# Performance work log

Measured on AMD Instinct MI355X. Metric: run time of the kernel, lower is better.

Reference implementation:

```python
import jax, jax.numpy as jnp
import numpy as np

N_NODES = 100000
N_EDGES = 1200000
IN_DIM, HID_DIM, OUT_DIM = 64, 64, 32


def setup_inputs() -> dict:
    key = jax.random.key(0)
    k1, k2, k3, k4, k5, k6 = jax.random.split(key, 6)
    x = jax.random.normal(k1, (N_NODES, IN_DIM), dtype=jnp.float32)
    edge_index = jax.random.randint(k2, (2, N_EDGES), 0, N_NODES, dtype=jnp.int64)
    # Glorot-style init for GCN linear weights
    W1 = jax.random.normal(k3, (IN_DIM, HID_DIM), dtype=jnp.float32) / np.sqrt(IN_DIM)
    b1 = jnp.zeros((HID_DIM,), dtype=jnp.float32)
    W2 = jax.random.normal(k4, (HID_DIM, OUT_DIM), dtype=jnp.float32) / np.sqrt(HID_DIM)
    b2 = jnp.zeros((OUT_DIM,), dtype=jnp.float32)
    return {"x": x, "edge_index": edge_index, "W1": W1, "b1": b1, "W2": W2, "b2": b2}


def _gcn_conv(x, W, b, src, dst, norm, n_nodes):
    # linear transform first (PyG GCNConv): [N, out]
    h = x @ W
    # gather messages along edges (incl. self-loops), scale by sym norm
    msg = h[src] * norm[:, None]            # [E+N, out]
    out = jax.ops.segment_sum(msg, dst, num_segments=n_nodes)
    return out + b


def reference(x, edge_index, W1, b1, W2, b2):
    n_nodes = x.shape[0]
    # add self-loops (PyG GCNConv default)
    loop = jnp.arange(n_nodes, dtype=edge_index.dtype)
    src = jnp.concatenate([edge_index[0], loop])
    dst = jnp.concatenate([edge_index[1], loop])
    # symmetric normalization: deg^{-1/2}[src] * deg^{-1/2}[dst]
    deg = jax.ops.segment_sum(jnp.ones_like(dst, dtype=x.dtype), dst, num_segments=n_nodes)
    deg_isqrt = jax.lax.rsqrt(deg)          # deg >= 1 due to self-loops
    norm = deg_isqrt[src] * deg_isqrt[dst]
    h = _gcn_conv(x, W1, b1, src, dst, norm, n_nodes)
    h = jax.nn.relu(h)
    out = _gcn_conv(h, W2, b2, src, dst, norm, n_nodes)
    return out
```

## Files before the change

kernel.cpp:

```cpp
#include <hip/hip_runtime.h>
#include <hip/hip_fp16.h>
#include <type_traits>

#define NBUCK 512

typedef _Float16 half8 __attribute__((ext_vector_type(8)));
typedef float floatx4 __attribute__((ext_vector_type(4)));

__device__ inline void unpack8(const float4& raw, float* f) {
    const __half2* p = (const __half2*)&raw;
#pragma unroll
    for (int i = 0; i < 4; ++i) {
        float2 t = __half22float2(p[i]);
        f[2 * i] = t.x;
        f[2 * i + 1] = t.y;
    }
}


__global__ void bucket_hist_kernel(const int* __restrict__ dst, int* __restrict__ bucketCnt,
                                   int E, int R) {
    __shared__ int h[NBUCK];
    int tid = threadIdx.x;
    for (int i = tid; i < NBUCK; i += blockDim.x) h[i] = 0;
    __syncthreads();
    for (int i = blockIdx.x * blockDim.x + tid; i < E; i += gridDim.x * blockDim.x)
        atomicAdd(&h[dst[i] / R], 1);
    __syncthreads();
    for (int i = tid; i < NBUCK; i += blockDim.x)
        if (h[i]) atomicAdd(&bucketCnt[i], h[i]);
}


__global__ void bucket_scan_kernel(const int* __restrict__ bucketCnt, int* __restrict__ bucketBase,
                                   int* __restrict__ bucketCursor) {
    __shared__ int lds[NBUCK];
    int tid = threadIdx.x;
    int v = bucketCnt[tid];
    lds[tid] = v;
    __syncthreads();
    for (int off = 1; off < NBUCK; off <<= 1) {
        int x = (tid >= off) ? lds[tid - off] : 0;
        __syncthreads();
        lds[tid] += x;
        __syncthreads();
    }
    int excl = lds[tid] - v;
    bucketBase[tid] = excl;
    bucketCursor[tid] = excl;
    if (tid == NBUCK - 1) bucketBase[NBUCK] = lds[tid];
}


__global__ __launch_bounds__(1024) void partition_kernel(const int* __restrict__ src,
                                                         const int* __restrict__ dst,
                                                         int* __restrict__ bucketCursor,
                                                         unsigned long long* __restrict__ pairs,
                                                         int E, int R) {
    __shared__ int h[NBUCK];
    __shared__ int base[NBUCK];
    __shared__ int lcur[NBUCK];
    const int CH = 16384;
    int start = blockIdx.x * CH;
    int count = E - start;
    if (count > CH) count = CH;
    int tid = threadIdx.x;
    if (tid < NBUCK) h[tid] = 0;
    __syncthreads();
    for (int i = tid; i < count; i += 1024)
        atomicAdd(&h[dst[start + i] / R], 1);
    __syncthreads();
    if (tid < NBUCK) {
        base[tid] = h[tid] ? atomicAdd(&bucketCursor[tid], h[tid]) : 0;
        lcur[tid] = 0;
    }
    __syncthreads();
    for (int i = tid; i < count; i += 1024) {
        int d = dst[start + i];
        int s = src[start + i];
        int b = d / R;
        int r = atomicAdd(&lcur[b], 1);
        pairs[base[b] + r] = ((unsigned long long)(unsigned)s << 32) | (unsigned)d;
    }
}


__global__ void bucket_csr_kernel(const unsigned long long* __restrict__ pairs,
                                  const int* __restrict__ bucketBase, int* __restrict__ counts,
                                  int* __restrict__ offs, float* __restrict__ dinv,
                                  int* __restrict__ ssrc, int N, int R) {
    __shared__ int h[256];
    __shared__ int loffs[256];
    __shared__ int cur[256];
    int b = blockIdx.x, tid = threadIdx.x;
    int nodeBase = b * R;
    int beg = bucketBase[b], end = bucketBase[b + 1];
    h[tid] = 0;
    __syncthreads();
    for (int i = beg + tid; i < end; i += 256) {
        int d = (int)(pairs[i] & 0xffffffffull);
        atomicAdd(&h[d - nodeBase], 1);
    }
    __syncthreads();
    int v = h[tid];
    loffs[tid] = v;
    __syncthreads();
    for (int off = 1; off < 256; off <<= 1) {
        int x = (tid >= off) ? loffs[tid - off] : 0;
        __syncthreads();
        loffs[tid] += x;
        __syncthreads();
    }
    int excl = loffs[tid] - v;
    cur[tid] = excl;
    int node = nodeBase + tid;
    if (tid < R && node < N) {
        counts[node] = v;
        offs[node] = beg + excl;
        dinv[node] = rsqrtf((float)v + 1.0f);
    }
    __syncthreads();
    for (int i = beg + tid; i < end; i += 256) {
        unsigned long long p = pairs[i];
        int d = (int)(p & 0xffffffffull);
        int s = (int)(p >> 32);
        int r = atomicAdd(&cur[d - nodeBase], 1);
        ssrc[beg + r] = s;
    }
}


template <int OUTD, typename TIN>
__global__ void gemm_mfma_kernel(const TIN* __restrict__ X, const float* __restrict__ W,
                                 __half* __restrict__ H, int M, int ntiles) {
    constexpr int NC = OUTD / 16;
    const int lane = threadIdx.x & 63;
    const int wid  = threadIdx.x >> 6;
    const int q    = lane >> 4;
    const int m    = lane & 15;

    half8 bfrag[2][NC];
#pragma unroll
    for (int s = 0; s < 2; ++s)
#pragma unroll
        for (int c = 0; c < NC; ++c)
#pragma unroll
            for (int j = 0; j < 8; ++j)
                bfrag[s][c][j] = (_Float16)W[(s * 32 + q * 8 + j) * OUTD + c * 16 + m];

    for (int tile = blockIdx.x * 4 + wid; tile < ntiles; tile += gridDim.x * 4) {
        int rowBase = tile * 16;
        int rowA = rowBase + m;
        if (rowA > M - 1) rowA = M - 1;

        half8 afrag[2];
        if constexpr (std::is_same<TIN, float>::value) {
            const float4* Xr = (const float4*)(X + (size_t)rowA * 64);
#pragma unroll
            for (int s = 0; s < 2; ++s) {
                float4 v0 = Xr[s * 8 + q * 2 + 0];
                float4 v1 = Xr[s * 8 + q * 2 + 1];
                afrag[s][0] = (_Float16)v0.x;
                afrag[s][1] = (_Float16)v0.y;
                afrag[s][2] = (_Float16)v0.z;
                afrag[s][3] = (_Float16)v0.w;
                afrag[s][4] = (_Float16)v1.x;
                afrag[s][5] = (_Float16)v1.y;
                afrag[s][6] = (_Float16)v1.z;
                afrag[s][7] = (_Float16)v1.w;
            }
        } else {
            const half8* Xr = (const half8*)(X + (size_t)rowA * 64);
#pragma unroll
            for (int s = 0; s < 2; ++s)
                afrag[s] = Xr[s * 4 + q];
        }

        floatx4 acc[NC];
#pragma unroll
        for (int c = 0; c < NC; ++c) acc[c] = (floatx4){0.f, 0.f, 0.f, 0.f};
#pragma unroll
        for (int s = 0; s < 2; ++s)
#pragma unroll
            for (int c = 0; c < NC; ++c)
                acc[c] = __builtin_amdgcn_mfma_f32_16x16x32_f16(afrag[s], bfrag[s][c], acc[c],
                                                                0, 0, 0);

#pragma unroll
        for (int r = 0; r < 4; ++r) {
            int row = rowBase + q * 4 + r;
            if (row < M) {
#pragma unroll
                for (int c = 0; c < NC; ++c)
                    H[(size_t)row * OUTD + c * 16 + m] = __float2half(acc[c][r]);
            }
        }
    }
}


__global__ __launch_bounds__(256) void agg64_kernel(
    const float4* __restrict__ hrow4, const int* __restrict__ ssrc,
    const int* __restrict__ offs, const int* __restrict__ counts,
    const float* __restrict__ dinv, const float* __restrict__ b1,
    float4* __restrict__ out4, int N) {
    int tid = threadIdx.x;
    int wid = tid >> 6, lane = tid & 63;
    int o = lane >> 3, l = lane & 7;
    int node = blockIdx.x * 4 + wid;
    if (node >= N) return;
    int beg = offs[node], cnt = counts[node];
    float a[8];
#pragma unroll
    for (int j = 0; j < 8; ++j) a[j] = 0.f;
    for (int base = 0; base < cnt; base += 64) {
        int rem = cnt - base;
        if (rem > 64) rem = 64;
        int idx = 0;
        float dv = 0.0f;
        if (lane < rem) {
            idx = ssrc[beg + base + lane];
            dv  = dinv[idx];
        }
        for (int k = 0; k < rem; k += 16) {
            int e0 = k + o;
            int e1 = k + 8 + o;
            int   s0  = __shfl(idx, e0, 64);
            float nv0 = __shfl(dv, e0, 64);
            int   s1  = __shfl(idx, e1, 64);
            float nv1 = __shfl(dv, e1, 64);
            float4 r0 = hrow4[(size_t)s0 * 8 + l];
            float4 r1 = hrow4[(size_t)s1 * 8 + l];
            float f0[8], f1[8];
            unpack8(r0, f0);
            unpack8(r1, f1);
#pragma unroll
            for (int j = 0; j < 8; ++j) a[j] = fmaf(f0[j], nv0, a[j]);
#pragma unroll
            for (int j = 0; j < 8; ++j) a[j] = fmaf(f1[j], nv1, a[j]);
        }
    }
#pragma unroll
    for (int m = 8; m < 64; m <<= 1) {
#pragma unroll
        for (int j = 0; j < 8; ++j) a[j] += __shfl_xor(a[j], m, 64);
    }
    if (o == 0) {
        float dd = dinv[node];
        float4 sraw = hrow4[(size_t)node * 8 + l];
        float sf[8];
        unpack8(sraw, sf);
        __half2 p[4];
#pragma unroll
        for (int i = 0; i < 4; ++i) {
            float rx = fmaxf(dd * (a[2 * i] + sf[2 * i] * dd) + b1[8 * l + 2 * i], 0.0f);
            float ry = fmaxf(dd * (a[2 * i + 1] + sf[2 * i + 1] * dd) + b1[8 * l + 2 * i + 1], 0.0f);
            p[i] = __floats2half2_rn(rx, ry);
        }
        out4[(size_t)node * 8 + l] = *(const float4*)p;
    }
}


__global__ __launch_bounds__(256) void agg32_kernel(
    const float4* __restrict__ hrow4, const int* __restrict__ ssrc,
    const int* __restrict__ offs, const int* __restrict__ counts,
    const float* __restrict__ dinv, const float* __restrict__ b2,
    float4* __restrict__ out4, int N) {
    int tid = threadIdx.x;
    int wid = tid >> 6, lane = tid & 63;
    int o = lane >> 2, l = lane & 3;
    int node = blockIdx.x * 4 + wid;
    if (node >= N) return;
    int beg = offs[node], cnt = counts[node];
    float a[8];
#pragma unroll
    for (int j = 0; j < 8; ++j) a[j] = 0.f;
    for (int base = 0; base < cnt; base += 64) {
        int rem = cnt - base;
        if (rem > 64) rem = 64;
        int idx = 0;
        float dv = 0.0f;
        if (lane < rem) {
            idx = ssrc[beg + base + lane];
            dv  = dinv[idx];
        }
        for (int k = 0; k < rem; k += 16) {
            int e = k + o;
            int   s  = __shfl(idx, e, 64);
            float nv = __shfl(dv, e, 64);
            float4 raw = hrow4[(size_t)s * 4 + l];
            float f[8];
            unpack8(raw, f);
#pragma unroll
            for (int j = 0; j < 8; ++j) a[j] = fmaf(f[j], nv, a[j]);
        }
    }
#pragma unroll
    for (int m = 4; m < 64; m <<= 1) {
#pragma unroll
        for (int j = 0; j < 8; ++j) a[j] += __shfl_xor(a[j], m, 64);
    }
    if (o == 0) {
        float dd = dinv[node];
        float4 sraw = hrow4[(size_t)node * 4 + l];
        float sf[8];
        unpack8(sraw, sf);
        float r[8];
#pragma unroll
        for (int j = 0; j < 8; ++j)
            r[j] = dd * (a[j] + sf[j] * dd) + b2[8 * l + j];
        out4[(size_t)node * 8 + 2 * l + 0] = make_float4(r[0], r[1], r[2], r[3]);
        out4[(size_t)node * 8 + 2 * l + 1] = make_float4(r[4], r[5], r[6], r[7]);
    }
}


extern "C" void kernel_launch(void* const* d_in, const int* in_sizes, int n_in,
                              void* d_out, int out_size, void* d_ws, size_t ws_size,
                              hipStream_t stream) {
    const float* x  = (const float*)d_in[0];
    const int*   ei = (const int*)d_in[1];
    const float* W1 = (const float*)d_in[2];
    const float* b1 = (const float*)d_in[3];
    const float* W2 = (const float*)d_in[4];
    const float* b2 = (const float*)d_in[5];
    float* out = (float*)d_out;

    const int N = in_sizes[0] / 64;
    const int E = in_sizes[1] / 2;
    const int* src = ei;
    const int* dst = ei + E;

    const int Npad = (N + 1023) & ~1023;
    const int R    = (N + NBUCK - 1) / NBUCK;

    unsigned long long* pairs = (unsigned long long*)d_ws;
    int*   ssrc   = (int*)(pairs + E);
    int*   counts = ssrc + E;
    int*   offs   = counts + Npad;
    float* dinv   = (float*)(offs + Npad);
    int*   bucketCnt    = (int*)(dinv + Npad);
    int*   bucketBase   = bucketCnt + NBUCK;
    int*   bucketCursor = bucketBase + NBUCK + 1;
    size_t hoff = (size_t)(bucketCursor + NBUCK + 1 - (int*)d_ws);
    hoff = (hoff + 3) & ~(size_t)3;
    __half* h    = (__half*)((int*)d_ws + hoff);
    __half* out1 = h + (size_t)N * 64;
    __half* h2   = h;

    const int T = 256;

    hipMemsetAsync(bucketCnt, 0, NBUCK * sizeof(int), stream);
    bucket_hist_kernel<<<512, T, 0, stream>>>(dst, bucketCnt, E, R);
    bucket_scan_kernel<<<1, NBUCK, 0, stream>>>(bucketCnt, bucketBase, bucketCursor);
    partition_kernel<<<(E + 16383) / 16384, 1024, 0, stream>>>(src, dst, bucketCursor, pairs, E, R);
    bucket_csr_kernel<<<NBUCK, T, 0, stream>>>(pairs, bucketBase, counts, offs, dinv, ssrc, N, R);

    const int ntiles = (N + 15) / 16;

    gemm_mfma_kernel<64, float><<<782, T, 0, stream>>>(x, W1, h, N, ntiles);
    agg64_kernel<<<(N + 3) / 4, T, 0, stream>>>((const float4*)h, ssrc, offs, counts, dinv, b1,
                                                (float4*)out1, N);

    gemm_mfma_kernel<32, __half><<<782, T, 0, stream>>>(out1, W2, h2, N, ntiles);
    agg32_kernel<<<(N + 3) / 4, T, 0, stream>>>((const float4*)h2, ssrc, offs, counts, dinv, b2,
                                                (float4*)out, N);
}
```

Before: 240.0 us.

## Map one node per lane-group instead of per wavefront in aggregation kernels

Both aggregation kernels now assign each destination node to a small lane group (8 lanes for 64-dim, 4 lanes for 32-dim) instead of a whole 64-lane wavefront. Each group loops over its edges in chunks equal to the group size, broadcasting indices within the group by shuffle. This removes the cross-lane xor reduction and the idle lanes caused by average degree (~13) being far below 64. In exchange, lanes in one wavefront diverge on different degree counts, and each group has fewer gathers in flight per node.

```diff
diff --git a/kernel.cpp b/kernel.cpp
--- a/kernel.cpp
+++ b/kernel.cpp
@@ -204,61 +204,47 @@
     const int* __restrict__ offs, const int* __restrict__ counts,
     const float* __restrict__ dinv, const float* __restrict__ b1,
     float4* __restrict__ out4, int N) {
-    int tid = threadIdx.x;
-    int wid = tid >> 6, lane = tid & 63;
-    int o = lane >> 3, l = lane & 7;
-    int node = blockIdx.x * 4 + wid;
+    int tid  = threadIdx.x;
+    int lane = tid & 63;
+    int l    = tid & 7;
+    int gb   = lane & 56;
+    int node = blockIdx.x * 32 + (tid >> 3);
     if (node >= N) return;
     int beg = offs[node], cnt = counts[node];
     float a[8];
 #pragma unroll
     for (int j = 0; j < 8; ++j) a[j] = 0.f;
-    for (int base = 0; base < cnt; base += 64) {
-        int rem = cnt - base;
-        if (rem > 64) rem = 64;
+    for (int base = 0; base < cnt; base += 8) {
+        int p = base + l;
         int idx = 0;
         float dv = 0.0f;
-        if (lane < rem) {
-            idx = ssrc[beg + base + lane];
+        if (p < cnt) {
+            idx = ssrc[beg + p];
             dv  = dinv[idx];
         }
-        for (int k = 0; k < rem; k += 16) {
-            int e0 = k + o;
-            int e1 = k + 8 + o;
-            int   s0  = __shfl(idx, e0, 64);
-            float nv0 = __shfl(dv, e0, 64);
-            int   s1  = __shfl(idx, e1, 64);
-            float nv1 = __shfl(dv, e1, 64);
-            float4 r0 = hrow4[(size_t)s0 * 8 + l];
-            float4 r1 = hrow4[(size_t)s1 * 8 + l];
-            float f0[8], f1[8];
-            unpack8(r0, f0);
-            unpack8(r1, f1);
-#pragma unroll
-            for (int j = 0; j < 8; ++j) a[j] = fmaf(f0[j], nv0, a[j]);
-#pragma unroll
-            for (int j = 0; j < 8; ++j) a[j] = fmaf(f1[j], nv1, a[j]);
-        }
-    }
-#pragma unroll
-    for (int m = 8; m < 64; m <<= 1) {
-#pragma unroll
-        for (int j = 0; j < 8; ++j) a[j] += __shfl_xor(a[j], m, 64);
-    }
-    if (o == 0) {
-        float dd = dinv[node];
-        float4 sraw = hrow4[(size_t)node * 8 + l];
-        float sf[8];
-        unpack8(sraw, sf);
-        __half2 p[4];
-#pragma unroll
-        for (int i = 0; i < 4; ++i) {
-            float rx = fmaxf(dd * (a[2 * i] + sf[2 * i] * dd) + b1[8 * l + 2 * i], 0.0f);
-            float ry = fmaxf(dd * (a[2 * i + 1] + sf[2 * i + 1] * dd) + b1[8 * l + 2 * i + 1], 0.0f);
-            p[i] = __floats2half2_rn(rx, ry);
-        }
-        out4[(size_t)node * 8 + l] = *(const float4*)p;
-    }
+#pragma unroll
+        for (int j = 0; j < 8; ++j) {
+            int   s  = __shfl(idx, gb | j, 64);
+            float nv = __shfl(dv, gb | j, 64);
+            float4 raw = hrow4[(size_t)s * 8 + l];
+            float f[8];
+            unpack8(raw, f);
+#pragma unroll
+            for (int d = 0; d < 8; ++d) a[d] = fmaf(f[d], nv, a[d]);
+        }
+    }
+    float dd = dinv[node];
+    float4 sraw = hrow4[(size_t)node * 8 + l];
+    float sf[8];
+    unpack8(sraw, sf);
+    __half2 pk[4];
+#pragma unroll
+    for (int i = 0; i < 4; ++i) {
+        float rx = fmaxf(dd * (a[2 * i] + sf[2 * i] * dd) + b1[8 * l + 2 * i], 0.0f);
+        float ry = fmaxf(dd * (a[2 * i + 1] + sf[2 * i + 1] * dd) + b1[8 * l + 2 * i + 1], 0.0f);
+        pk[i] = __floats2half2_rn(rx, ry);
+    }
+    out4[(size_t)node * 8 + l] = *(const float4*)pk;
 }
 
 
@@ -267,52 +253,45 @@
     const int* __restrict__ offs, const int* __restrict__ counts,
     const float* __restrict__ dinv, const float* __restrict__ b2,
     float4* __restrict__ out4, int N) {
-    int tid = threadIdx.x;
-    int wid = tid >> 6, lane = tid & 63;
-    int o = lane >> 2, l = lane & 3;
-    int node = blockIdx.x * 4 + wid;
+    int tid  = threadIdx.x;
+    int lane = tid & 63;
+    int l    = tid & 3;
+    int gb   = lane & 60;
+    int node = blockIdx.x * 64 + (tid >> 2);
     if (node >= N) return;
     int beg = offs[node], cnt = counts[node];
     float a[8];
 #pragma unroll
     for (int j = 0; j < 8; ++j) a[j] = 0.f;
-    for (int base = 0; base < cnt; base += 64) {
-        int rem = cnt - base;
-        if (rem > 64) rem = 64;
+    for (int base = 0; base < cnt; base += 4) {
+        int p = base + l;
         int idx = 0;
         float dv = 0.0f;
-        if (lane < rem) {
-            idx = ssrc[beg + base + lane];
+        if (p < cnt) {
+            idx = ssrc[beg + p];
             dv  = dinv[idx];
         }
-        for (int k = 0; k < rem; k += 16) {
-            int e = k + o;
-            int   s  = __shfl(idx, e, 64);
-            float nv = __shfl(dv, e, 64);
+#pragma unroll
+        for (int j = 0; j < 4; ++j) {
+            int   s  = __shfl(idx, gb | j, 64);
+            float nv = __shfl(dv, gb | j, 64);
             float4 raw = hrow4[(size_t)s * 4 + l];
             float f[8];
             unpack8(raw, f);
 #pragma unroll
-            for (int j = 0; j < 8; ++j) a[j] = fmaf(f[j], nv, a[j]);
-        }
-    }
-#pragma unroll
-    for (int m = 4; m < 64; m <<= 1) {
-#pragma unroll
-        for (int j = 0; j < 8; ++j) a[j] += __shfl_xor(a[j], m, 64);
-    }
-    if (o == 0) {
-        float dd = dinv[node];
-        float4 sraw = hrow4[(size_t)node * 4 + l];
-        float sf[8];
-        unpack8(sraw, sf);
-        float r[8];
-#pragma unroll
-        for (int j = 0; j < 8; ++j)
-            r[j] = dd * (a[j] + sf[j] * dd) + b2[8 * l + j];
-        out4[(size_t)node * 8 + 2 * l + 0] = make_float4(r[0], r[1], r[2], r[3]);
-        out4[(size_t)node * 8 + 2 * l + 1] = make_float4(r[4], r[5], r[6], r[7]);
-    }
+            for (int d = 0; d < 8; ++d) a[d] = fmaf(f[d], nv, a[d]);
+        }
+    }
+    float dd = dinv[node];
+    float4 sraw = hrow4[(size_t)node * 4 + l];
+    float sf[8];
+    unpack8(sraw, sf);
+    float r[8];
+#pragma unroll
+    for (int j = 0; j < 8; ++j)
+        r[j] = dd * (a[j] + sf[j] * dd) + b2[8 * l + j];
+    out4[(size_t)node * 8 + 2 * l + 0] = make_float4(r[0], r[1], r[2], r[3]);
+    out4[(size_t)node * 8 + 2 * l + 1] = make_float4(r[4], r[5], r[6], r[7]);
 }
 
 
@@ -360,10 +339,10 @@
     const int ntiles = (N + 15) / 16;
 
     gemm_mfma_kernel<64, float><<<782, T, 0, stream>>>(x, W1, h, N, ntiles);
-    agg64_kernel<<<(N + 3) / 4, T, 0, stream>>>((const float4*)h, ssrc, offs, counts, dinv, b1,
-                                                (float4*)out1, N);
+    agg64_kernel<<<(N + 31) / 32, T, 0, stream>>>((const float4*)h, ssrc, offs, counts, dinv, b1,
+                                                  (float4*)out1, N);
 
     gemm_mfma_kernel<32, __half><<<782, T, 0, stream>>>(out1, W2, h2, N, ntiles);
-    agg32_kernel<<<(N + 3) / 4, T, 0, stream>>>((const float4*)h2, ssrc, offs, counts, dinv, b2,
-                                                (float4*)out, N);
-}
+    agg32_kernel<<<(N + 63) / 64, T, 0, stream>>>((const float4*)h2, ssrc, offs, counts, dinv, b2,
+                                                  (float4*)out, N);
+}
```

Result: faster. 220.1 us (-8.3%).
